# Optimization experiments

Measured on AMD Instinct MI355X. Metric: run time of the kernel, lower is better.

The kernel has to match this reference:

```python
import jax, jax.numpy as jnp
import numpy as np

N, SEQ, HID, ENC, E = 16384, 512, 1024, 256, 8


def setup_inputs() -> dict:
    key = jax.random.key(0)
    ks = jax.random.split(key, 8)
    def w(k, shape, fan_in):
        return jax.random.normal(k, shape, dtype=jnp.float32) * (1.0 / np.sqrt(fan_in))
    return {
        "x": jax.random.normal(ks[0], (N, SEQ), dtype=jnp.float32),
        "ids": jax.random.randint(ks[1], (N,), 0, E),
        "W1": w(ks[2], (SEQ, HID), SEQ),
        "b1": jnp.zeros((HID,), jnp.float32),
        "W2": w(ks[3], (HID, ENC), HID),
        "b2": jnp.zeros((ENC,), jnp.float32),
        "W3": w(ks[4], (E, ENC, HID), ENC),
        "b3": jnp.zeros((E, HID), jnp.float32),
        "W4": w(ks[5], (E, HID, SEQ), HID),
        "b4": jnp.zeros((E, SEQ), jnp.float32),
    }


def reference(x, ids, W1, b1, W2, b2, W3, b3, W4, b4):
    # fixed trunk (shared across all combination IDs)
    h = jax.nn.relu(x @ W1 + b1)          # [N, HID]
    z = jax.nn.relu(h @ W2 + b2)          # [N, ENC]
    # per-combination expert head: Linear(enc,hid)+ReLU+Linear(hid,seq)
    n_experts = W3.shape[0]
    oh = jax.nn.one_hot(ids, n_experts, dtype=x.dtype)  # [N, E] row->expert mask
    y = jnp.zeros((x.shape[0], W4.shape[-1]), dtype=x.dtype)
    for e in range(n_experts):  # small fixed expert count; each iter is a big GEMM
        u = jax.nn.relu(z @ W3[e] + b3[e])             # [N, HID]
        y = y + (u @ W4[e] + b4[e]) * oh[:, e:e + 1]   # scatter-back via mask
    return y
```

## Files before the change

kernel.cpp:

```cpp
#include <hip/hip_runtime.h>
#include <hip/hip_bf16.h>

#define NROWS 16384
#define SEQD  512
#define HIDD  1024
#define ENCD  256
#define NEXP  8
#define NBLK  64
#define MAXTILES 136
#define MPAD_MAX (MAXTILES * 128)

using bf16 = __hip_bfloat16;
typedef __bf16 bf16x8 __attribute__((ext_vector_type(8)));
typedef float  f32x4  __attribute__((ext_vector_type(4)));

__device__ __forceinline__ int xcd_swz(int bx, int gx) {
  const int cpx = gx >> 3;
  return (bx & 7) * cpx + (bx >> 3);
}

enum : size_t {
  OFF_XB   = 0,
  OFF_W1T  = OFF_XB  + (size_t)NROWS * SEQD * 2,
  OFF_W2T  = OFF_W1T + (size_t)HIDD * SEQD * 2,
  OFF_H    = OFF_W2T + (size_t)ENCD * HIDD * 2,
  OFF_W3T  = OFF_H   + (size_t)NROWS * HIDD * 2,
  OFF_W4T  = OFF_W3T + (size_t)NEXP * HIDD * ENCD * 2,
  OFF_Z    = OFF_W4T + (size_t)NEXP * SEQD * HIDD * 2,
  OFF_PERM = OFF_Z   + (size_t)NROWS * ENCD * 2,
  OFF_META = OFF_PERM + (size_t)MPAD_MAX * 4,
  OFF_U    = 0,
  WS_NEED  = OFF_META + 8192
};

__device__ __forceinline__ void gload_lds16(const void* g, void* l) {
  __builtin_amdgcn_global_load_lds(
      (const __attribute__((address_space(1))) void*)g,
      (__attribute__((address_space(3))) void*)l, 16, 0, 0);
}

__global__ void prep_k(const float* __restrict__ x,
                       const float* __restrict__ W1, const float* __restrict__ W2,
                       const float* __restrict__ W3, const float* __restrict__ W4,
                       const int* __restrict__ ids,
                       bf16* __restrict__ Xb, bf16* __restrict__ W1t,
                       bf16* __restrict__ W2t, bf16* __restrict__ W3t,
                       bf16* __restrict__ W4t, int* __restrict__ gh) {
  __shared__ float t[32][33];
  int b = blockIdx.x;
  const int tid = threadIdx.x;
  if (b < 4096) {
    size_t i = (size_t)b * 256 + tid;
    float4 a = ((const float4*)x)[i * 2];
    float4 c = ((const float4*)x)[i * 2 + 1];
    __align__(16) bf16 v[8] = {
      __float2bfloat16(a.x), __float2bfloat16(a.y), __float2bfloat16(a.z), __float2bfloat16(a.w),
      __float2bfloat16(c.x), __float2bfloat16(c.y), __float2bfloat16(c.z), __float2bfloat16(c.w)};
    *(int4*)(Xb + i * 8) = *(const int4*)v;
    return;
  }
  b -= 4096;
  if (b >= 6912) {
    __shared__ int c[NEXP];
    if (tid < NEXP) c[tid] = 0;
    __syncthreads();
    atomicAdd(&c[ids[(b - 6912) * 256 + tid]], 1);
    __syncthreads();
    if (tid < NEXP) gh[(b - 6912) * NEXP + tid] = c[tid];
    return;
  }
  const float* s; bf16* d; int R, C;
  if (b < 512)              { s = W1; d = W1t; R = SEQD; C = HIDD; }
  else if ((b -= 512) < 256){ s = W2; d = W2t; R = HIDD; C = ENCD; }
  else if ((b -= 256) < 2048){
    int z = b >> 8; b &= 255; s = W3 + (size_t)z * ENCD * HIDD; d = W3t + (size_t)z * ENCD * HIDD;
    R = ENCD; C = HIDD;
  } else {
    b -= 2048; int z = b >> 9; b &= 511;
    s = W4 + (size_t)z * HIDD * SEQD; d = W4t + (size_t)z * HIDD * SEQD;
    R = HIDD; C = SEQD;
  }
  const int nbx = C >> 5;
  const int bx = (b % nbx) * 32, by = (b / nbx) * 32;
  const int tx = tid & 31, ty = tid >> 5;
  #pragma unroll
  for (int i = 0; i < 32; i += 8) t[ty + i][tx] = s[(size_t)(by + ty + i) * C + bx + tx];
  __syncthreads();
  #pragma unroll
  for (int i = 0; i < 32; i += 8)
    d[(size_t)(bx + ty + i) * R + by + tx] = __float2bfloat16(t[tx][ty + i]);
}


__global__ __launch_bounds__(1024) void bases_k(int* __restrict__ meta,
                                                int* __restrict__ perm) {
  int* gh        = meta;
  int* bases     = meta + 512;
  int* blockbase = meta + 528;
  __shared__ int counts[NEXP];
  __shared__ int base_s[NEXP + 1];
  const int tid = threadIdx.x;
  if (tid < NEXP) {
    int s = 0;
    for (int b = 0; b < NBLK; ++b) s += gh[b * NEXP + tid];
    counts[tid] = s;
  }
  __syncthreads();
  if (tid == 0) {
    int t = 0;
    for (int e = 0; e < NEXP; ++e) { base_s[e] = t; t += (counts[e] + 127) & ~127; }
    base_s[NEXP] = t;
  }
  __syncthreads();
  if (tid < NEXP) {
    int run = base_s[tid];
    for (int b = 0; b < NBLK; ++b) { blockbase[b * NEXP + tid] = run; run += gh[b * NEXP + tid]; }
  }
  if (tid == 0)
    for (int e = 0; e <= NEXP; ++e) bases[e] = base_s[e];
  #pragma unroll
  for (int e = 0; e < NEXP; ++e) {
    int lo = base_s[e] + counts[e];
    int i  = lo + tid;
    if (i < base_s[e + 1]) perm[i] = -1;
  }
}

__global__ void scatter_k(const int* __restrict__ ids, const int* __restrict__ blockbase,
                          int* __restrict__ perm) {
  __shared__ int wavehist[4][NEXP];
  const int tid = threadIdx.x, w = tid >> 6, lane = tid & 63;
  const int n = blockIdx.x * 256 + tid;
  const int e = ids[n];
  const unsigned long long lt = (1ull << lane) - 1ull;
  int myrank = 0;
  #pragma unroll
  for (int ee = 0; ee < NEXP; ++ee) {
    unsigned long long bb = __ballot(e == ee);
    if (ee == e) myrank = __popcll(bb & lt);
    if (lane == 0) wavehist[w][ee] = __popcll(bb);
  }
  __syncthreads();
  int pre = 0;
  for (int w2 = 0; w2 < w; ++w2) pre += wavehist[w2][e];
  perm[blockbase[blockIdx.x * NEXP + e] + pre + myrank] = n;
}

template <bool GATHER_A, bool EXPERT, bool RELU, bool SCATTER_F32, int NSLOTS>
__global__ __launch_bounds__(256, (NSLOTS == 2 ? 2 : 1)) void gemm128(
    const bf16* __restrict__ A, const bf16* __restrict__ Bt,
    const float* __restrict__ bias, void* __restrict__ Out,
    int Ncols, int K, const int* __restrict__ perm, const int* __restrict__ bases) {
  __shared__ char lds[NSLOTS * 32768];

  const int tid  = threadIdx.x;
  const int wid  = tid >> 6;
  const int lane = tid & 63;
  const int lm = lane & 15, l4 = lane >> 4;
  const int wm = wid >> 1, wn = wid & 1;

  const int tileM = xcd_swz(blockIdx.x, gridDim.x), tileN = blockIdx.y;
  int expert = 0;
  if (EXPERT) {
    const int total = bases[8];
    if (tileM * 128 >= total) return;
    const int r0 = tileM * 128;
    #pragma unroll
    for (int e = 1; e < NEXP; ++e) expert += (r0 >= bases[e]) ? 1 : 0;
    Bt   += (size_t)expert * Ncols * K;
    bias += expert * Ncols;
  }
  const int row0 = tileM * 128, col0 = tileN * 128;

  const bf16* gA[4];
  const bf16* gB[4];
  #pragma unroll
  for (int i = 0; i < 4; ++i) {
    int flat = (i * 4 + wid) * 1024 + lane * 16;
    int r    = flat >> 7;
    int cb   = (flat & 127) ^ ((r & 7) << 4);
    int arow;
    if (GATHER_A) {
      int p = perm[row0 + r];
      arow = (p < 0) ? 0 : p;
    } else {
      arow = row0 + r;
    }
    gA[i] = A  + (size_t)arow * K + (cb >> 1);
    gB[i] = Bt + (size_t)(col0 + r) * K + (cb >> 1);
  }

  f32x4 acc[4][4];
  #pragma unroll
  for (int i = 0; i < 4; ++i)
    #pragma unroll
    for (int j = 0; j < 4; ++j) { f32x4 z = {0.f, 0.f, 0.f, 0.f}; acc[i][j] = z; }

  int aoff[4], boff[4];
  const int swz = (lm & 7) << 4;
  #pragma unroll
  for (int i = 0; i < 4; ++i) {
    int ar = wm * 64 + i * 16 + lm;
    aoff[i] = ar * 128 + ((l4 * 16) ^ swz);
    int br = wn * 64 + i * 16 + lm;
    boff[i] = br * 128 + ((l4 * 16) ^ swz);
  }

  const int nk = K >> 6;
  asm volatile("s_waitcnt vmcnt(0)" ::: "memory");
  __builtin_amdgcn_sched_barrier(0);

  #pragma unroll
  for (int s = 0; s < NSLOTS; ++s) {
    if (s < nk) {
      #pragma unroll
      for (int i = 0; i < 4; ++i) {
        gload_lds16(gA[i] + (size_t)s * 64, lds + s * 32768 + (i * 4 + wid) * 1024);
        gload_lds16(gB[i] + (size_t)s * 64, lds + s * 32768 + 16384 + (i * 4 + wid) * 1024);
      }
    }
  }

  int slot = 0;
  for (int kt = 0; kt < nk; ++kt) {
    int inflight = nk - 1 - kt;
    if (inflight > NSLOTS - 1) inflight = NSLOTS - 1;
    if (inflight >= 2)      asm volatile("s_waitcnt vmcnt(16)" ::: "memory");
    else if (inflight == 1) asm volatile("s_waitcnt vmcnt(8)"  ::: "memory");
    else                    asm volatile("s_waitcnt vmcnt(0)"  ::: "memory");
    asm volatile("s_barrier" ::: "memory");
    __builtin_amdgcn_sched_barrier(0);

    const char* Ac = lds + slot * 32768;
    const char* Bc = Ac + 16384;
    #pragma unroll
    for (int kk = 0; kk < 2; ++kk) {
      bf16x8 af[4], bfr[4];
      #pragma unroll
      for (int i = 0; i < 4; ++i) af[i]  = *(const bf16x8*)(Ac + (aoff[i] ^ (kk * 64)));
      #pragma unroll
      for (int i = 0; i < 4; ++i) bfr[i] = *(const bf16x8*)(Bc + (boff[i] ^ (kk * 64)));
      #pragma unroll
      for (int mi = 0; mi < 4; ++mi)
        #pragma unroll
        for (int ni = 0; ni < 4; ++ni)
          acc[mi][ni] = __builtin_amdgcn_mfma_f32_16x16x32_bf16(af[mi], bfr[ni], acc[mi][ni], 0, 0, 0);
    }

    asm volatile("s_barrier" ::: "memory");
    __builtin_amdgcn_sched_barrier(0);
    if (kt + NSLOTS < nk) {
      char* An = lds + slot * 32768;
      #pragma unroll
      for (int i = 0; i < 4; ++i) {
        gload_lds16(gA[i] + (size_t)(kt + NSLOTS) * 64, An + (i * 4 + wid) * 1024);
        gload_lds16(gB[i] + (size_t)(kt + NSLOTS) * 64, An + 16384 + (i * 4 + wid) * 1024);
      }
    }
    slot = (slot + 1 == NSLOTS) ? 0 : slot + 1;
  }

  float bv[4];
  #pragma unroll
  for (int ni = 0; ni < 4; ++ni) bv[ni] = bias[col0 + wn * 64 + ni * 16 + lm];
  #pragma unroll
  for (int mi = 0; mi < 4; ++mi) {
    #pragma unroll
    for (int r = 0; r < 4; ++r) {
      int rowp = row0 + wm * 64 + mi * 16 + l4 * 4 + r;
      int orow = rowp;
      bool valid = true;
      if (SCATTER_F32) {
        int p = perm[rowp];
        valid = (p >= 0);
        orow  = valid ? p : 0;
      }
      #pragma unroll
      for (int ni = 0; ni < 4; ++ni) {
        float v = acc[mi][ni][r] + bv[ni];
        if (RELU) v = v > 0.f ? v : 0.f;
        int n = col0 + wn * 64 + ni * 16 + lm;
        if (SCATTER_F32) {
          if (valid) ((float*)Out)[(size_t)orow * Ncols + n] = v;
        } else {
          ((bf16*)Out)[(size_t)rowp * Ncols + n] = __float2bfloat16(v);
        }
      }
    }
  }
}

__global__ __launch_bounds__(512, 2) void gemm256p(
    const bf16* __restrict__ A, const bf16* __restrict__ Bt,
    const float* __restrict__ bias, bf16* __restrict__ Out, int Ncols, int K) {
  __shared__ char lds[131072];

  const int tid  = threadIdx.x;
  const int wid  = tid >> 6;
  const int lane = tid & 63;
  const int lm = lane & 15, l4 = lane >> 4;
  const int wm = wid >> 2, wn = wid & 3;
  const int tileM = xcd_swz(blockIdx.x, gridDim.x);
  const int row0 = tileM * 256, col0 = blockIdx.y * 256;

  const bf16* gA[4];
  const bf16* gB[4];
  #pragma unroll
  for (int i = 0; i < 4; ++i) {
    const int flat = i * 8192 + tid * 16;
    const int r    = flat >> 7;
    const int cb   = (flat & 127) ^ ((r & 7) << 4);
    gA[i] = A  + (size_t)(row0 + r) * K + (cb >> 1);
    gB[i] = Bt + (size_t)(col0 + r) * K + (cb >> 1);
  }

  f32x4 acc[8][4];
  #pragma unroll
  for (int i = 0; i < 8; ++i)
    #pragma unroll
    for (int j = 0; j < 4; ++j) { f32x4 z = {0.f, 0.f, 0.f, 0.f}; acc[i][j] = z; }

  int aoff[2][4], boff[2][2];
  #pragma unroll
  for (int h = 0; h < 2; ++h)
    #pragma unroll
    for (int q = 0; q < 4; ++q) {
      int row = wm * 128 + h * 64 + q * 16 + lm;
      aoff[h][q] = row * 128 + ((l4 * 16) ^ ((row & 7) << 4));
    }
  #pragma unroll
  for (int nh = 0; nh < 2; ++nh)
    #pragma unroll
    for (int p = 0; p < 2; ++p) {
      int row = wn * 64 + nh * 32 + p * 16 + lm;
      boff[nh][p] = row * 128 + ((l4 * 16) ^ ((row & 7) << 4));
    }

  const int nk = K >> 6;
  asm volatile("s_waitcnt vmcnt(0)" ::: "memory");
  __builtin_amdgcn_sched_barrier(0);

  #pragma unroll
  for (int i = 0; i < 4; ++i) {
    gload_lds16(gA[i], lds + i * 8192 + tid * 16);
    gload_lds16(gB[i], lds + 32768 + i * 8192 + tid * 16);
  }
  #pragma unroll
  for (int i = 0; i < 4; ++i) {
    gload_lds16(gA[i] + 64, lds + 65536 + i * 8192 + tid * 16);
    gload_lds16(gB[i] + 64, lds + 65536 + 32768 + i * 8192 + tid * 16);
  }
  asm volatile("s_waitcnt vmcnt(8)" ::: "memory");
  asm volatile("s_barrier" ::: "memory");
  __builtin_amdgcn_sched_barrier(0);

  bf16x8 a[4][2], b[2][2];
  #pragma unroll
  for (int q = 0; q < 4; ++q)
    #pragma unroll
    for (int kk = 0; kk < 2; ++kk) a[q][kk] = *(const bf16x8*)(lds + (aoff[0][q] ^ (kk * 64)));
  #pragma unroll
  for (int p = 0; p < 2; ++p)
    #pragma unroll
    for (int kk = 0; kk < 2; ++kk) b[p][kk] = *(const bf16x8*)(lds + 32768 + (boff[0][p] ^ (kk * 64)));

#define MFMA16(MOFF, NOFF)                                                      \
  __builtin_amdgcn_s_setprio(1);                                                \
  _Pragma("unroll")                                                             \
  for (int kk = 0; kk < 2; ++kk)                                                \
    _Pragma("unroll")                                                           \
    for (int mf = 0; mf < 4; ++mf)                                              \
      _Pragma("unroll")                                                         \
      for (int nf = 0; nf < 2; ++nf)                                            \
        acc[MOFF + mf][NOFF + nf] = __builtin_amdgcn_mfma_f32_16x16x32_bf16(    \
            a[mf][kk], b[nf][kk], acc[MOFF + mf][NOFF + nf], 0, 0, 0);          \
  __builtin_amdgcn_s_setprio(0);

#define RD_A(H, BUFA)                                                           \
  _Pragma("unroll")                                                             \
  for (int q = 0; q < 4; ++q)                                                   \
    _Pragma("unroll")                                                           \
    for (int kk = 0; kk < 2; ++kk)                                              \
      a[q][kk] = *(const bf16x8*)((BUFA) + (aoff[H][q] ^ (kk * 64)));
#define RD_B(NH, BUFB)                                                          \
  _Pragma("unroll")                                                             \
  for (int p = 0; p < 2; ++p)                                                   \
    _Pragma("unroll")                                                           \
    for (int kk = 0; kk < 2; ++kk)                                              \
      b[p][kk] = *(const bf16x8*)((BUFB) + (boff[NH][p] ^ (kk * 64)));

  for (int kt = 0; kt < nk; ++kt) {
    const char* bufA = lds + (kt & 1) * 65536;
    const char* bufB = bufA + 32768;
    asm volatile("s_barrier" ::: "memory");
    MFMA16(0, 0)
    RD_B(1, bufB)
    asm volatile("s_barrier" ::: "memory");
    MFMA16(0, 2)
    RD_A(1, bufA)
    asm volatile("s_barrier" ::: "memory");
    MFMA16(4, 2)
    RD_B(0, bufB)
    asm volatile("s_barrier" ::: "memory");
    MFMA16(4, 0)
    if (kt + 1 < nk) {
      asm volatile("s_waitcnt lgkmcnt(0)" ::: "memory");
      asm volatile("s_barrier" ::: "memory");
      __builtin_amdgcn_sched_barrier(0);
      if (kt + 2 < nk) {
        char* sA = lds + (kt & 1) * 65536;
        #pragma unroll
        for (int i = 0; i < 4; ++i) {
          gload_lds16(gA[i] + (size_t)(kt + 2) * 64, sA + i * 8192 + tid * 16);
          gload_lds16(gB[i] + (size_t)(kt + 2) * 64, sA + 32768 + i * 8192 + tid * 16);
        }
        asm volatile("s_waitcnt vmcnt(8)" ::: "memory");
      } else {
        asm volatile("s_waitcnt vmcnt(0)" ::: "memory");
      }
      __builtin_amdgcn_sched_barrier(0);
      const char* nA = lds + ((kt + 1) & 1) * 65536;
      const char* nB = nA + 32768;
      RD_A(0, nA)
      RD_B(0, nB)
    }
  }
#undef MFMA16
#undef RD_A
#undef RD_B

  float bv[4];
  #pragma unroll
  for (int nf = 0; nf < 4; ++nf) bv[nf] = bias[col0 + wn * 64 + nf * 16 + lm];
  #pragma unroll
  for (int mf = 0; mf < 8; ++mf) {
    #pragma unroll
    for (int rr = 0; rr < 4; ++rr) {
      const int rowp = row0 + wm * 128 + mf * 16 + l4 * 4 + rr;
      #pragma unroll
      for (int nf = 0; nf < 4; ++nf) {
        float v = acc[mf][nf][rr] + bv[nf];
        v = v > 0.f ? v : 0.f;
        Out[(size_t)rowp * Ncols + col0 + wn * 64 + nf * 16 + lm] = __float2bfloat16(v);
      }
    }
  }
}

extern "C" void kernel_launch(void* const* d_in, const int* in_sizes, int n_in,
                              void* d_out, int out_size, void* d_ws, size_t ws_size,
                              hipStream_t stream) {
  const float* x  = (const float*)d_in[0];
  const int*   ids= (const int*)d_in[1];
  const float* W1 = (const float*)d_in[2];
  const float* b1 = (const float*)d_in[3];
  const float* W2 = (const float*)d_in[4];
  const float* b2 = (const float*)d_in[5];
  const float* W3 = (const float*)d_in[6];
  const float* b3 = (const float*)d_in[7];
  const float* W4 = (const float*)d_in[8];
  const float* b4 = (const float*)d_in[9];

  char* ws = (char*)d_ws;
  bf16* Xb  = (bf16*)(ws + OFF_XB);
  bf16* W1t = (bf16*)(ws + OFF_W1T);
  bf16* W2t = (bf16*)(ws + OFF_W2T);
  bf16* W3t = (bf16*)(ws + OFF_W3T);
  bf16* W4t = (bf16*)(ws + OFF_W4T);
  bf16* H   = (bf16*)(ws + OFF_H);
  bf16* Z   = (bf16*)(ws + OFF_Z);
  bf16* U   = (bf16*)(ws + OFF_U);
  int*  perm      = (int*)(ws + OFF_PERM);
  int*  meta      = (int*)(ws + OFF_META);
  int*  gh        = meta;
  int*  bases     = meta + 512;
  int*  blockbase = meta + 528;

  prep_k<<<dim3(11072), dim3(256), 0, stream>>>(x, W1, W2, W3, W4, ids,
                                                Xb, W1t, W2t, W3t, W4t, gh);
  bases_k  <<<dim3(1),    dim3(1024), 0, stream>>>(meta, perm);
  scatter_k<<<dim3(NBLK), dim3(256), 0, stream>>>(ids, blockbase, perm);

  gemm256p<<<dim3(NROWS / 256, HIDD / 256), dim3(512), 0, stream>>>(
      Xb, W1t, b1, H, HIDD, SEQD);
  gemm128<false, false, true, false, 3><<<dim3(NROWS / 128, ENCD / 128), dim3(256), 0, stream>>>(
      H, W2t, b2, Z, ENCD, HIDD, nullptr, nullptr);
  gemm128<true, true, true, false, 2><<<dim3(MAXTILES, HIDD / 128), dim3(256), 0, stream>>>(
      Z, W3t, b3, U, HIDD, ENCD, perm, bases);
  gemm128<false, true, false, true, 2><<<dim3(MAXTILES, SEQD / 128), dim3(256), 0, stream>>>(
      U, W4t, b4, d_out, SEQD, HIDD, perm, bases);

  (void)in_sizes; (void)n_in; (void)out_size; (void)ws_size;
}
```

Measured before the change: 114.7 us.

## Fold expert routing bases and scatter into first trunk GEMM launch

Removes the separate single-block bases kernel and the scatter kernel, and runs their work in an extra grid row (blockIdx.y==4) of the first trunk GEMM. Each of the 64 extra blocks recomputes its own expert prefix from the global histogram, and block 0 writes the bases and pads perm with -1. This drops two serialized launches and their dependency bubbles. In exchange the work is recomputed redundantly per block, and the 131 KB LDS allocation of the GEMM kernel also applies to these light blocks.

After: 113.8 us (median of 3 runs). About the same (-0.8%).

```diff
diff --git a/kernel.cpp b/kernel.cpp
--- a/kernel.cpp
+++ b/kernel.cpp
@@ -91,61 +91,6 @@
     d[(size_t)(bx + ty + i) * R + by + tx] = __float2bfloat16(t[tx][ty + i]);
 }
 
-
-__global__ __launch_bounds__(1024) void bases_k(int* __restrict__ meta,
-                                                int* __restrict__ perm) {
-  int* gh        = meta;
-  int* bases     = meta + 512;
-  int* blockbase = meta + 528;
-  __shared__ int counts[NEXP];
-  __shared__ int base_s[NEXP + 1];
-  const int tid = threadIdx.x;
-  if (tid < NEXP) {
-    int s = 0;
-    for (int b = 0; b < NBLK; ++b) s += gh[b * NEXP + tid];
-    counts[tid] = s;
-  }
-  __syncthreads();
-  if (tid == 0) {
-    int t = 0;
-    for (int e = 0; e < NEXP; ++e) { base_s[e] = t; t += (counts[e] + 127) & ~127; }
-    base_s[NEXP] = t;
-  }
-  __syncthreads();
-  if (tid < NEXP) {
-    int run = base_s[tid];
-    for (int b = 0; b < NBLK; ++b) { blockbase[b * NEXP + tid] = run; run += gh[b * NEXP + tid]; }
-  }
-  if (tid == 0)
-    for (int e = 0; e <= NEXP; ++e) bases[e] = base_s[e];
-  #pragma unroll
-  for (int e = 0; e < NEXP; ++e) {
-    int lo = base_s[e] + counts[e];
-    int i  = lo + tid;
-    if (i < base_s[e + 1]) perm[i] = -1;
-  }
-}
-
-__global__ void scatter_k(const int* __restrict__ ids, const int* __restrict__ blockbase,
-                          int* __restrict__ perm) {
-  __shared__ int wavehist[4][NEXP];
-  const int tid = threadIdx.x, w = tid >> 6, lane = tid & 63;
-  const int n = blockIdx.x * 256 + tid;
-  const int e = ids[n];
-  const unsigned long long lt = (1ull << lane) - 1ull;
-  int myrank = 0;
-  #pragma unroll
-  for (int ee = 0; ee < NEXP; ++ee) {
-    unsigned long long bb = __ballot(e == ee);
-    if (ee == e) myrank = __popcll(bb & lt);
-    if (lane == 0) wavehist[w][ee] = __popcll(bb);
-  }
-  __syncthreads();
-  int pre = 0;
-  for (int w2 = 0; w2 < w; ++w2) pre += wavehist[w2][e];
-  perm[blockbase[blockIdx.x * NEXP + e] + pre + myrank] = n;
-}
-
 template <bool GATHER_A, bool EXPERT, bool RELU, bool SCATTER_F32, int NSLOTS>
 __global__ __launch_bounds__(256, (NSLOTS == 2 ? 2 : 1)) void gemm128(
     const bf16* __restrict__ A, const bf16* __restrict__ Bt,
@@ -292,10 +237,67 @@
 
 __global__ __launch_bounds__(512, 2) void gemm256p(
     const bf16* __restrict__ A, const bf16* __restrict__ Bt,
-    const float* __restrict__ bias, bf16* __restrict__ Out, int Ncols, int K) {
+    const float* __restrict__ bias, bf16* __restrict__ Out, int Ncols, int K,
+    const int* __restrict__ ids, const int* __restrict__ gh,
+    int* __restrict__ perm, int* __restrict__ bases_g) {
   __shared__ char lds[131072];
 
   const int tid  = threadIdx.x;
+
+  if (blockIdx.y == 4) {
+    __shared__ int counts_s[NEXP];
+    __shared__ int base_s[NEXP + 1];
+    __shared__ int myb[NEXP];
+    __shared__ int wavehist[4][NEXP];
+    const int bx = blockIdx.x;
+    if (tid < NEXP) {
+      int s = 0, run = 0;
+      for (int b = 0; b < NBLK; ++b) {
+        int g = gh[b * NEXP + tid];
+        if (b < bx) run += g;
+        s += g;
+      }
+      counts_s[tid] = s;
+      myb[tid] = run;
+    }
+    __syncthreads();
+    if (tid == 0) {
+      int t = 0;
+      for (int e = 0; e < NEXP; ++e) { base_s[e] = t; t += (counts_s[e] + 127) & ~127; }
+      base_s[NEXP] = t;
+    }
+    __syncthreads();
+    if (tid < NEXP) myb[tid] += base_s[tid];
+    if (bx == 0) {
+      if (tid <= NEXP) bases_g[tid] = base_s[tid];
+      #pragma unroll
+      for (int e = 0; e < NEXP; ++e) {
+        int i = base_s[e] + counts_s[e] + tid;
+        if (i < base_s[e + 1]) perm[i] = -1;
+      }
+    }
+    __syncthreads();
+    const int w = tid >> 6, lane = tid & 63;
+    const unsigned long long lt = (1ull << lane) - 1ull;
+    int e = 0, myrank = 0;
+    if (w < 4) {
+      e = ids[bx * 256 + tid];
+      #pragma unroll
+      for (int ee = 0; ee < NEXP; ++ee) {
+        unsigned long long bb = __ballot(e == ee);
+        if (ee == e) myrank = __popcll(bb & lt);
+        if (lane == 0) wavehist[w][ee] = __popcll(bb);
+      }
+    }
+    __syncthreads();
+    if (w < 4) {
+      int pre = 0;
+      for (int w2 = 0; w2 < w; ++w2) pre += wavehist[w2][e];
+      perm[myb[e] + pre + myrank] = bx * 256 + tid;
+    }
+    return;
+  }
+
   const int wid  = tid >> 6;
   const int lane = tid & 63;
   const int lm = lane & 15, l4 = lane >> 4;
@@ -470,19 +472,16 @@
   bf16* H   = (bf16*)(ws + OFF_H);
   bf16* Z   = (bf16*)(ws + OFF_Z);
   bf16* U   = (bf16*)(ws + OFF_U);
-  int*  perm      = (int*)(ws + OFF_PERM);
-  int*  meta      = (int*)(ws + OFF_META);
-  int*  gh        = meta;
-  int*  bases     = meta + 512;
-  int*  blockbase = meta + 528;
+  int*  perm  = (int*)(ws + OFF_PERM);
+  int*  meta  = (int*)(ws + OFF_META);
+  int*  gh    = meta;
+  int*  bases = meta + 512;
 
   prep_k<<<dim3(11072), dim3(256), 0, stream>>>(x, W1, W2, W3, W4, ids,
                                                 Xb, W1t, W2t, W3t, W4t, gh);
-  bases_k  <<<dim3(1),    dim3(1024), 0, stream>>>(meta, perm);
-  scatter_k<<<dim3(NBLK), dim3(256), 0, stream>>>(ids, blockbase, perm);
-
-  gemm256p<<<dim3(NROWS / 256, HIDD / 256), dim3(512), 0, stream>>>(
-      Xb, W1t, b1, H, HIDD, SEQD);
+
+  gemm256p<<<dim3(NROWS / 256, HIDD / 256 + 1), dim3(512), 0, stream>>>(
+      Xb, W1t, b1, H, HIDD, SEQD, ids, gh, perm, bases);
   gemm128<false, false, true, false, 3><<<dim3(NROWS / 128, ENCD / 128), dim3(256), 0, stream>>>(
       H, W2t, b2, Z, ENCD, HIDD, nullptr, nullptr);
   gemm128<true, true, true, false, 2><<<dim3(MAXTILES, HIDD / 128), dim3(256), 0, stream>>>(
```
